# Performance work log

Hardware: AMD Instinct MI355X
Metric: run time of the kernel (lower is better)

Reference implementation:

```python
import jax, jax.numpy as jnp
import numpy as np

N = 50000      # total nodes (features)
E = 150000     # total directed edges (incl. padding row 0 semantics of original)
NB = 8         # MAX_NB
H = 128        # hidden_size
FF = 40        # FEATURE_FDIM
EF = 1         # EDGE_FDIM
B = 500        # molecules in batch
DEPTH = 6


def setup_inputs() -> dict:
    key = jax.random.key(0)
    ks = jax.random.split(key, 8)
    features = jax.random.normal(ks[0], (N, FF), jnp.float32)
    fedges = jax.random.normal(ks[1], (E, FF + EF), jnp.float32)
    agraph = jax.random.randint(ks[2], (N, NB), 0, E, dtype=jnp.int32)
    egraph = jax.random.randint(ks[3], (E, NB), 0, E, dtype=jnp.int32)
    # contiguous per-molecule scopes: (start, length), uniform 100 nodes each
    L = N // B
    starts = jnp.arange(B, dtype=jnp.int32) * L
    lens = jnp.full((B,), L, dtype=jnp.int32)
    scope = jnp.stack([starts, lens], axis=1)
    # Dense weights (Glorot-ish scale); W_i and W_h have no bias, W_o has bias
    W_i = jax.random.normal(ks[4], (FF + EF, H), jnp.float32) / np.sqrt(FF + EF)
    W_h = jax.random.normal(ks[5], (H, H), jnp.float32) / np.sqrt(H)
    W_o = jax.random.normal(ks[6], (FF + H, H), jnp.float32) / np.sqrt(FF + H)
    b_o = jnp.zeros((H,), jnp.float32)
    return {"features": features, "fedges": fedges, "agraph": agraph,
            "egraph": egraph, "scope": scope, "W_i": W_i, "W_h": W_h,
            "W_o": W_o, "b_o": b_o}


def reference(features, fedges, agraph, egraph, scope, W_i, W_h, W_o, b_o):
    # binput: [E, H]; message: [E, H]
    binput = fedges @ W_i
    message = jax.nn.sigmoid(binput)
    for _ in range(DEPTH - 1):
        # gather neighbor edge messages [E, NB, H], sum over NB
        nei = jnp.sum(message[egraph], axis=1)
        message = jax.nn.sigmoid(binput + nei @ W_h)
    # per-node aggregation of incoming edge messages [N, H]
    nei = jnp.sum(message[agraph], axis=1)
    ainput = jnp.concatenate([features, nei], axis=1)        # [N, FF+H]
    feature_hiddens = jax.nn.sigmoid(ainput @ W_o + b_o)    # [N, H]
    # ragged per-molecule mean over contiguous scopes
    lens = scope[:, 1]
    mol_ids = jnp.repeat(jnp.arange(B), lens, total_repeat_length=N)
    sums = jax.ops.segment_sum(feature_hiddens, mol_ids, num_segments=B)
    mol_vecs = sums / lens[:, None].astype(feature_hiddens.dtype)
    return mol_vecs
```

## Files before the change

kernel.cpp:

```cpp
#include <hip/hip_runtime.h>


typedef __attribute__((ext_vector_type(4))) float f32x4;
typedef __attribute__((ext_vector_type(2))) float f32x2;
typedef __attribute__((ext_vector_type(8))) short s16x8;
typedef unsigned short u16;
typedef unsigned char u8;

constexpr int Nn   = 50000;
constexpr int Ee   = 150000;
constexpr int NBn  = 8;
constexpr int Hh   = 128;
constexpr int FFn  = 40;
constexpr int Bm   = 500;
constexpr int ITERS = 5;
constexpr int KP   = 136;
constexpr int KI   = 72;
constexpr int KO   = 200;
constexpr int ACCW = 132;
constexpr int ACC2 = 130;

__device__ __forceinline__ float sigmoidf_(float x) {
    return 1.0f / (1.0f + __expf(-x));
}
__device__ __forceinline__ u16 f2bf(float f) {
    unsigned u = __float_as_uint(f);
    u += 0x7fffu + ((u >> 16) & 1u);
    return (u16)(u >> 16);
}
__device__ __forceinline__ float bflo(unsigned u) { return __uint_as_float(u << 16); }
__device__ __forceinline__ float bfhi(unsigned u) { return __uint_as_float(u & 0xffff0000u); }
__device__ __forceinline__ float bf1(u16 h) { return __uint_as_float(((unsigned)h) << 16); }
__device__ __forceinline__ unsigned pack2(float x, float y) {
    return (unsigned)f2bf(x) | ((unsigned)f2bf(y) << 16);
}
__device__ __forceinline__ void add8f8(float* a, uint2 v) {
    f32x2 p;
    p = __builtin_amdgcn_cvt_pk_f32_fp8((int)v.x, false); a[0] += p[0]; a[1] += p[1];
    p = __builtin_amdgcn_cvt_pk_f32_fp8((int)v.x, true);  a[2] += p[0]; a[3] += p[1];
    p = __builtin_amdgcn_cvt_pk_f32_fp8((int)v.y, false); a[4] += p[0]; a[5] += p[1];
    p = __builtin_amdgcn_cvt_pk_f32_fp8((int)v.y, true);  a[6] += p[0]; a[7] += p[1];
}
__device__ __forceinline__ unsigned pack4f8(float a, float b, float c, float d) {
    int r = 0;
    r = __builtin_amdgcn_cvt_pk_fp8_f32(a, b, r, false);
    r = __builtin_amdgcn_cvt_pk_fp8_f32(c, d, r, true);
    return (unsigned)r;
}

__global__ __launch_bounds__(256) void k_prep1(
    const float* __restrict__ W_h, const float* __restrict__ W_i,
    u16* __restrict__ wt_h, u16* __restrict__ wt_i)
{
    int i = blockIdx.x * 256 + threadIdx.x;
    if (i < Hh * Hh) {
        int f = i >> 9, l = (i >> 3) & 63, e = i & 7;
        int ks = f >> 3, c = f & 7;
        int k = ks * 32 + (l >> 4) * 8 + e, n = c * 16 + (l & 15);
        wt_h[i] = f2bf(W_h[k * Hh + n]);
    } else {
        int j = i - Hh * Hh;
        if (j < 16 * 512) {
            int f = j >> 9, l = (j >> 3) & 63, e = j & 7;
            int ks = f >> 3, c = f & 7;
            int k = ks * 32 + (l >> 4) * 8 + e, n = c * 16 + (l & 15);
            wt_i[j] = (k < 41) ? f2bf(W_i[k * Hh + n]) : (u16)0;
        }
    }
}

__global__ __launch_bounds__(256) void k_prep2(
    const float* __restrict__ W_o, u16* __restrict__ wt_o)
{
    int i = blockIdx.x * 256 + threadIdx.x;
    if (i < 48 * 512) {
        int f = i >> 9, l = (i >> 3) & 63, e = i & 7;
        int ks = f >> 3, c = f & 7;
        int k = ks * 32 + (l >> 4) * 8 + e, n = c * 16 + (l & 15);
        u16 v = 0;
        if (k < FFn)                 v = f2bf(W_o[k * Hh + n]);
        else if (k >= 64 && k < 192) v = f2bf(W_o[(k - 24) * Hh + n]);
        wt_o[i] = v;
    }
}

union BinSmem {
    struct { u16 Wi[16 * 512]; u16 A[Hh * KI]; } s;
    float acc[Hh][ACCW];
};

__global__ __launch_bounds__(512, 4) void k_binput(
    const float* __restrict__ fedges, const u16* __restrict__ wt_i,
    u16* __restrict__ binput_bf, u8* __restrict__ msg)
{
    __shared__ BinSmem u;
    const int t = threadIdx.x;
    const int row0 = blockIdx.x * 128;
    const int nvalid = min(128, Ee - row0);

    {
        uint4 z = make_uint4(0, 0, 0, 0);
        for (int i = t; i < Hh * KI / 8; i += 512) {
            if (i < 1024) ((uint4*)u.s.Wi)[i] = ((const uint4*)wt_i)[i];
            ((uint4*)u.s.A)[i] = z;
        }
    }
    __syncthreads();
    for (int i = t; i < nvalid * 41; i += 512) {
        int r = i / 41, k = i - r * 41;
        u.s.A[r * KI + k] = f2bf(fedges[(size_t)row0 * 41 + i]);
    }
    __syncthreads();

    const int lane = t & 63, wid = t >> 6, l15 = lane & 15, l4 = lane >> 4;
    f32x4 acc[8];
    #pragma unroll
    for (int b = 0; b < 8; ++b) acc[b] = (f32x4){0.f, 0.f, 0.f, 0.f};

    #pragma unroll
    for (int ks = 0; ks < 2; ++ks) {
        s16x8 a = *(const s16x8*)&u.s.A[(wid * 16 + l15) * KI + ks * 32 + l4 * 8];
        #pragma unroll
        for (int c = 0; c < 8; ++c) {
            s16x8 b = ((const s16x8*)u.s.Wi)[(ks * 8 + c) * 64 + lane];
            acc[c] = __builtin_amdgcn_mfma_f32_16x16x32_bf16(a, b, acc[c], 0, 0, 0);
        }
    }
    __syncthreads();

    #pragma unroll
    for (int c = 0; c < 8; ++c)
        #pragma unroll
        for (int j = 0; j < 4; ++j)
            u.acc[wid * 16 + l4 * 4 + j][c * 16 + l15] = acc[c][j];
    __syncthreads();

    for (int i = t; i < Hh * 16; i += 512) {
        int row = i >> 4, seg = i & 15, grow = row0 + row;
        if (grow < Ee) {
            float4 a0 = *(const float4*)&u.acc[row][seg * 8];
            float4 a1 = *(const float4*)&u.acc[row][seg * 8 + 4];
            size_t o = (size_t)grow * Hh + seg * 8;
            uint4 bv;
            bv.x = pack2(a0.x, a0.y); bv.y = pack2(a0.z, a0.w);
            bv.z = pack2(a1.x, a1.y); bv.w = pack2(a1.z, a1.w);
            *(uint4*)&binput_bf[o] = bv;
            uint2 m;
            m.x = pack4f8(sigmoidf_(a0.x), sigmoidf_(a0.y),
                          sigmoidf_(a0.z), sigmoidf_(a0.w));
            m.y = pack4f8(sigmoidf_(a1.x), sigmoidf_(a1.y),
                          sigmoidf_(a1.z), sigmoidf_(a1.w));
            *(uint2*)&msg[o] = m;
        }
    }
}

union IterSmem {
    u16 N[Hh * KP];
    float acc[64][ACC2];
};

__global__ __launch_bounds__(512, 6) void k_iter(
    const u8* __restrict__ msg_in, const int* __restrict__ egraph,
    const u16* __restrict__ wt_h, const u16* __restrict__ binput_bf,
    u8* __restrict__ msg_out)
{
    __shared__ IterSmem u;
    __shared__ int sEG[128 * NBn];
    const int t = threadIdx.x;
    const int row0 = blockIdx.x * 128;
    const int lane = t & 63, wid = t >> 6, l15 = lane & 15, l4 = lane >> 4;

    if (t < 256) {
        int r = row0 + (t >> 1);
        int4 v = make_int4(0, 0, 0, 0);
        if (r < Ee) v = ((const int4*)egraph)[r * 2 + (t & 1)];
        ((int4*)sEG)[t] = v;
    }
    __syncthreads();

    {
        const int s = t & 15, rl = t >> 4;
        #pragma unroll 2
        for (int pass = 0; pass < 4; ++pass) {
            int r = pass * 32 + rl;
            int grow = row0 + r;
            float a[8] = {0.f, 0.f, 0.f, 0.f, 0.f, 0.f, 0.f, 0.f};
            if (grow < Ee) {
                #pragma unroll
                for (int j = 0; j < NBn; ++j) {
                    int idx = sEG[r * NBn + j];
                    uint2 v = *(const uint2*)(msg_in + (size_t)idx * Hh + s * 8);
                    add8f8(a, v);
                }
            }
            uint4 o;
            o.x = pack2(a[0], a[1]); o.y = pack2(a[2], a[3]);
            o.z = pack2(a[4], a[5]); o.w = pack2(a[6], a[7]);
            *(uint4*)&u.N[r * KP + s * 8] = o;
        }
    }
    __syncthreads();

    f32x4 acc[8];
    #pragma unroll
    for (int b = 0; b < 8; ++b) acc[b] = (f32x4){0.f, 0.f, 0.f, 0.f};
    #pragma unroll
    for (int ks = 0; ks < 4; ++ks) {
        s16x8 a = *(const s16x8*)&u.N[(wid * 16 + l15) * KP + ks * 32 + l4 * 8];
        #pragma unroll
        for (int c = 0; c < 8; ++c) {
            s16x8 b = ((const s16x8*)wt_h)[(ks * 8 + c) * 64 + lane];
            acc[c] = __builtin_amdgcn_mfma_f32_16x16x32_bf16(a, b, acc[c], 0, 0, 0);
        }
    }
    __syncthreads();

    #pragma unroll
    for (int h = 0; h < 2; ++h) {
        if ((wid >> 2) == h) {
            #pragma unroll
            for (int c = 0; c < 8; ++c)
                #pragma unroll
                for (int j = 0; j < 4; ++j)
                    u.acc[(wid & 3) * 16 + l4 * 4 + j][c * 16 + l15] = acc[c][j];
        }
        __syncthreads();
        for (int i = t; i < 64 * 16; i += 512) {
            int r = i >> 4, seg = i & 15;
            int g = row0 + h * 64 + r;
            if (g < Ee) {
                float4 a0 = *(const float4*)&u.acc[r][seg * 8];
                float4 a1 = *(const float4*)&u.acc[r][seg * 8 + 4];
                size_t o = (size_t)g * Hh + seg * 8;
                uint4 bv = *(const uint4*)&binput_bf[o];
                uint2 m;
                m.x = pack4f8(sigmoidf_(a0.x + bflo(bv.x)), sigmoidf_(a0.y + bfhi(bv.x)),
                              sigmoidf_(a0.z + bflo(bv.y)), sigmoidf_(a0.w + bfhi(bv.y)));
                m.y = pack4f8(sigmoidf_(a1.x + bflo(bv.z)), sigmoidf_(a1.y + bfhi(bv.z)),
                              sigmoidf_(a1.z + bflo(bv.w)), sigmoidf_(a1.w + bfhi(bv.w)));
                *(uint2*)&msg_out[o] = m;
            }
        }
        __syncthreads();
    }
}

union FinSmem {
    u16 A[64 * KO];
    float acc[64][ACCW];
};

__global__ __launch_bounds__(256, 4) void k_final(
    const u8* __restrict__ msg_in, const int* __restrict__ agraph,
    const float* __restrict__ features, const u16* __restrict__ wt_o,
    const float* __restrict__ b_o, u16* __restrict__ hidden)
{
    __shared__ FinSmem u;
    __shared__ int sAG[64 * NBn];
    __shared__ float sBias[Hh];
    const int t = threadIdx.x;
    const int row0 = blockIdx.x * 64;
    const int nvalid = min(64, Nn - row0);

    {
        uint4 z = make_uint4(0, 0, 0, 0);
        for (int i = t; i < 64 * KO / 8; i += 256) ((uint4*)u.A)[i] = z;
    }
    if (t < 128) {
        int r = row0 + (t >> 1);
        int4 v = make_int4(0, 0, 0, 0);
        if (r < Nn) v = ((const int4*)agraph)[r * 2 + (t & 1)];
        ((int4*)sAG)[t] = v;
    }
    if (t < Hh / 4) ((float4*)sBias)[t] = ((const float4*)b_o)[t];
    __syncthreads();

    for (int i = t; i < nvalid * FFn; i += 256) {
        int r = i / FFn, k = i - r * FFn;
        u.A[r * KO + k] = f2bf(features[(size_t)row0 * FFn + i]);
    }
    {
        const int s = t & 15, rl = t >> 4;
        #pragma unroll 2
        for (int pass = 0; pass < 4; ++pass) {
            int r = pass * 16 + rl;
            int grow = row0 + r;
            float a[8] = {0.f, 0.f, 0.f, 0.f, 0.f, 0.f, 0.f, 0.f};
            if (grow < Nn) {
                #pragma unroll
                for (int j = 0; j < NBn; ++j) {
                    int idx = sAG[r * NBn + j];
                    uint2 v = *(const uint2*)(msg_in + (size_t)idx * Hh + s * 8);
                    add8f8(a, v);
                }
            }
            uint4 o;
            o.x = pack2(a[0], a[1]); o.y = pack2(a[2], a[3]);
            o.z = pack2(a[4], a[5]); o.w = pack2(a[6], a[7]);
            *(uint4*)&u.A[r * KO + 64 + s * 8] = o;
        }
    }
    __syncthreads();

    const int lane = t & 63, wid = t >> 6, l15 = lane & 15, l4 = lane >> 4;
    f32x4 acc[8];
    #pragma unroll
    for (int b = 0; b < 8; ++b) acc[b] = (f32x4){0.f, 0.f, 0.f, 0.f};

    #pragma unroll
    for (int ks = 0; ks < 6; ++ks) {
        s16x8 a = *(const s16x8*)&u.A[(wid * 16 + l15) * KO + ks * 32 + l4 * 8];
        #pragma unroll
        for (int c = 0; c < 8; ++c) {
            s16x8 b = ((const s16x8*)wt_o)[(ks * 8 + c) * 64 + lane];
            acc[c] = __builtin_amdgcn_mfma_f32_16x16x32_bf16(a, b, acc[c], 0, 0, 0);
        }
    }
    __syncthreads();

    #pragma unroll
    for (int c = 0; c < 8; ++c)
        #pragma unroll
        for (int j = 0; j < 4; ++j)
            u.acc[wid * 16 + l4 * 4 + j][c * 16 + l15] = acc[c][j];
    __syncthreads();

    for (int i = t; i < 64 * 16; i += 256) {
        int r = i >> 4, seg = i & 15, g = row0 + r;
        if (g < Nn) {
            float4 a0 = *(const float4*)&u.acc[r][seg * 8];
            float4 a1 = *(const float4*)&u.acc[r][seg * 8 + 4];
            const float* bb = &sBias[seg * 8];
            uint4 m;
            m.x = pack2(sigmoidf_(a0.x + bb[0]), sigmoidf_(a0.y + bb[1]));
            m.y = pack2(sigmoidf_(a0.z + bb[2]), sigmoidf_(a0.w + bb[3]));
            m.z = pack2(sigmoidf_(a1.x + bb[4]), sigmoidf_(a1.y + bb[5]));
            m.w = pack2(sigmoidf_(a1.z + bb[6]), sigmoidf_(a1.w + bb[7]));
            *(uint4*)&hidden[(size_t)g * Hh + seg * 8] = m;
        }
    }
}

__global__ __launch_bounds__(128) void k_pool(
    const u16* __restrict__ hidden, const int* __restrict__ scope,
    float* __restrict__ out)
{
    const int b = blockIdx.x;
    const int t = threadIdx.x;
    const int start = scope[b * 2 + 0];
    const int len   = scope[b * 2 + 1];
    float acc = 0.f;
    for (int i = 0; i < len; ++i)
        acc += bf1(hidden[(size_t)(start + i) * Hh + t]);
    out[(size_t)b * Hh + t] = acc / (float)len;
}

extern "C" void kernel_launch(void* const* d_in, const int* in_sizes, int n_in,
                              void* d_out, int out_size, void* d_ws, size_t ws_size,
                              hipStream_t stream)
{
    const float* features = (const float*)d_in[0];
    const float* fedges   = (const float*)d_in[1];
    const int*   agraph   = (const int*)d_in[2];
    const int*   egraph   = (const int*)d_in[3];
    const int*   scope    = (const int*)d_in[4];
    const float* W_i      = (const float*)d_in[5];
    const float* W_h      = (const float*)d_in[6];
    const float* W_o      = (const float*)d_in[7];
    const float* b_o      = (const float*)d_in[8];
    float* out = (float*)d_out;

    const size_t plane = (size_t)Ee * Hh;
    u16* binput_bf = (u16*)d_ws;
    u8*  msg0 = (u8*)(binput_bf + plane);
    u8*  msg1 = msg0 + plane;
    u16* wt_h = (u16*)(msg1 + plane);
    u16* wt_i = (u16*)msg1;
    u16* wt_o = binput_bf;

    k_prep1<<<(Hh * Hh + 16 * 512 + 255) / 256, 256, 0, stream>>>(W_h, W_i, wt_h, wt_i);

    const int eblocks = (Ee + 127) / 128;
    k_binput<<<eblocks, 512, 0, stream>>>(fedges, wt_i, binput_bf, msg0);

    u8* src = msg0;
    u8* dst = msg1;
    for (int d = 0; d < ITERS; ++d) {
        k_iter<<<eblocks, 512, 0, stream>>>(src, egraph, wt_h, binput_bf, dst);
        u8* tmp = src; src = dst; dst = tmp;
    }
    k_prep2<<<(48 * 512) / 256, 256, 0, stream>>>(W_o, wt_o);

    u16* hidden = (u16*)dst;
    const int nblocks = (Nn + 63) / 64;
    k_final<<<nblocks, 256, 0, stream>>>(src, agraph, features, wt_o, b_o, hidden);

    k_pool<<<Bm, 128, 0, stream>>>(hidden, scope, out);
}
```

Baseline: 293.0 us.

## Shrink k_iter to 64-row blocks with 16-byte gathers and direct egraph loads

```diff
diff --git a/kernel.cpp b/kernel.cpp
--- a/kernel.cpp
+++ b/kernel.cpp
@@ -40,6 +40,10 @@
     p = __builtin_amdgcn_cvt_pk_f32_fp8((int)v.x, true);  a[2] += p[0]; a[3] += p[1];
     p = __builtin_amdgcn_cvt_pk_f32_fp8((int)v.y, false); a[4] += p[0]; a[5] += p[1];
     p = __builtin_amdgcn_cvt_pk_f32_fp8((int)v.y, true);  a[6] += p[0]; a[7] += p[1];
+}
+__device__ __forceinline__ void add16f8(float* a, uint4 v) {
+    add8f8(a,     make_uint2(v.x, v.y));
+    add8f8(a + 8, make_uint2(v.z, v.w));
 }
 __device__ __forceinline__ unsigned pack4f8(float a, float b, float c, float d) {
     int r = 0;
@@ -156,48 +160,51 @@
 }
 
 union IterSmem {
-    u16 N[Hh * KP];
-    float acc[64][ACC2];
+    u16 N[64 * KP];
+    float acc[32][ACC2];
 };
 
-__global__ __launch_bounds__(512, 6) void k_iter(
+__global__ __launch_bounds__(256, 8) void k_iter(
     const u8* __restrict__ msg_in, const int* __restrict__ egraph,
     const u16* __restrict__ wt_h, const u16* __restrict__ binput_bf,
     u8* __restrict__ msg_out)
 {
     __shared__ IterSmem u;
-    __shared__ int sEG[128 * NBn];
     const int t = threadIdx.x;
-    const int row0 = blockIdx.x * 128;
+    const int row0 = blockIdx.x * 64;
     const int lane = t & 63, wid = t >> 6, l15 = lane & 15, l4 = lane >> 4;
 
-    if (t < 256) {
-        int r = row0 + (t >> 1);
-        int4 v = make_int4(0, 0, 0, 0);
-        if (r < Ee) v = ((const int4*)egraph)[r * 2 + (t & 1)];
-        ((int4*)sEG)[t] = v;
-    }
-    __syncthreads();
-
     {
-        const int s = t & 15, rl = t >> 4;
-        #pragma unroll 2
-        for (int pass = 0; pass < 4; ++pass) {
+        const int s = t & 7, rl = t >> 3;
+        #pragma unroll
+        for (int pass = 0; pass < 2; ++pass) {
             int r = pass * 32 + rl;
             int grow = row0 + r;
-            float a[8] = {0.f, 0.f, 0.f, 0.f, 0.f, 0.f, 0.f, 0.f};
+            float a[16];
+            #pragma unroll
+            for (int i = 0; i < 16; ++i) a[i] = 0.f;
             if (grow < Ee) {
-                #pragma unroll
-                for (int j = 0; j < NBn; ++j) {
-                    int idx = sEG[r * NBn + j];
-                    uint2 v = *(const uint2*)(msg_in + (size_t)idx * Hh + s * 8);
-                    add8f8(a, v);
-                }
+                int4 q0 = ((const int4*)egraph)[grow * 2];
+                int4 q1 = ((const int4*)egraph)[grow * 2 + 1];
+                const u8* bp = msg_in + (size_t)s * 16;
+                uint4 v0 = *(const uint4*)(bp + (size_t)q0.x * Hh);
+                uint4 v1 = *(const uint4*)(bp + (size_t)q0.y * Hh);
+                uint4 v2 = *(const uint4*)(bp + (size_t)q0.z * Hh);
+                uint4 v3 = *(const uint4*)(bp + (size_t)q0.w * Hh);
+                uint4 v4 = *(const uint4*)(bp + (size_t)q1.x * Hh);
+                uint4 v5 = *(const uint4*)(bp + (size_t)q1.y * Hh);
+                uint4 v6 = *(const uint4*)(bp + (size_t)q1.z * Hh);
+                uint4 v7 = *(const uint4*)(bp + (size_t)q1.w * Hh);
+                add16f8(a, v0); add16f8(a, v1); add16f8(a, v2); add16f8(a, v3);
+                add16f8(a, v4); add16f8(a, v5); add16f8(a, v6); add16f8(a, v7);
             }
-            uint4 o;
-            o.x = pack2(a[0], a[1]); o.y = pack2(a[2], a[3]);
-            o.z = pack2(a[4], a[5]); o.w = pack2(a[6], a[7]);
-            *(uint4*)&u.N[r * KP + s * 8] = o;
+            uint4 o0, o1;
+            o0.x = pack2(a[0],  a[1]);  o0.y = pack2(a[2],  a[3]);
+            o0.z = pack2(a[4],  a[5]);  o0.w = pack2(a[6],  a[7]);
+            o1.x = pack2(a[8],  a[9]);  o1.y = pack2(a[10], a[11]);
+            o1.z = pack2(a[12], a[13]); o1.w = pack2(a[14], a[15]);
+            *(uint4*)&u.N[r * KP + s * 16]     = o0;
+            *(uint4*)&u.N[r * KP + s * 16 + 8] = o1;
         }
     }
     __syncthreads();
@@ -218,17 +225,17 @@
 
     #pragma unroll
     for (int h = 0; h < 2; ++h) {
-        if ((wid >> 2) == h) {
+        if ((wid >> 1) == h) {
             #pragma unroll
             for (int c = 0; c < 8; ++c)
                 #pragma unroll
                 for (int j = 0; j < 4; ++j)
-                    u.acc[(wid & 3) * 16 + l4 * 4 + j][c * 16 + l15] = acc[c][j];
+                    u.acc[(wid & 1) * 16 + l4 * 4 + j][c * 16 + l15] = acc[c][j];
         }
         __syncthreads();
-        for (int i = t; i < 64 * 16; i += 512) {
+        for (int i = t; i < 32 * 16; i += 256) {
             int r = i >> 4, seg = i & 15;
-            int g = row0 + h * 64 + r;
+            int g = row0 + h * 32 + r;
             if (g < Ee) {
                 float4 a0 = *(const float4*)&u.acc[r][seg * 8];
                 float4 a1 = *(const float4*)&u.acc[r][seg * 8 + 4];
@@ -381,13 +388,13 @@
 
     k_prep1<<<(Hh * Hh + 16 * 512 + 255) / 256, 256, 0, stream>>>(W_h, W_i, wt_h, wt_i);
 
-    const int eblocks = (Ee + 127) / 128;
-    k_binput<<<eblocks, 512, 0, stream>>>(fedges, wt_i, binput_bf, msg0);
-
+    k_binput<<<(Ee + 127) / 128, 512, 0, stream>>>(fedges, wt_i, binput_bf, msg0);
+
+    const int eblocks64 = (Ee + 63) / 64;
     u8* src = msg0;
     u8* dst = msg1;
     for (int d = 0; d < ITERS; ++d) {
-        k_iter<<<eblocks, 512, 0, stream>>>(src, egraph, wt_h, binput_bf, dst);
+        k_iter<<<eblocks64, 256, 0, stream>>>(src, egraph, wt_h, binput_bf, dst);
         u8* tmp = src; src = dst; dst = tmp;
     }
     k_prep2<<<(48 * 512) / 256, 256, 0, stream>>>(W_o, wt_o);
```

After: 835.4 us. 2.85x slower.
